# Optimization experiments

Hardware: AMD Instinct MI355X
Metric: run time of the kernel (lower is better)

## Reference

```python
import jax, jax.numpy as jnp
import numpy as np

EMBED_DIM = 64
CODEBOOK_SIZE = 1024
BETA = 0.25


def setup_inputs() -> dict:
    key = jax.random.key(0)
    k1, k2 = jax.random.split(key)
    inputs = jax.random.normal(k1, (32, 4096, EMBED_DIM), dtype=jnp.float32)
    lim = 1.0 / CODEBOOK_SIZE
    codebook = jax.random.uniform(k2, (CODEBOOK_SIZE, EMBED_DIM),
                                  minval=-lim, maxval=lim, dtype=jnp.float32)
    return {"inputs": inputs, "codebook": codebook}


def reference(inputs, codebook):
    orig_shape = inputs.shape
    flat = inputs.reshape(-1, EMBED_DIM)  # [N, D]
    d = (jnp.sum(flat * flat, axis=1, keepdims=True)
         - 2.0 * flat @ codebook.T
         + jnp.sum(codebook * codebook, axis=1)[None, :])
    codes = jnp.argmin(d, axis=1)                      # [N]
    quantized = codebook[codes].reshape(orig_shape)    # gather + reshape
    straight_through = inputs + jax.lax.stop_gradient(quantized - inputs)
    commitment = jnp.mean((inputs - jax.lax.stop_gradient(quantized)) ** 2)
    codebook_loss = jnp.mean((quantized - jax.lax.stop_gradient(inputs)) ** 2)
    loss = codebook_loss + BETA * commitment
    return straight_through, codes.reshape(orig_shape[:-1]), loss
```

## Files before the change

kernel.cpp:

```cpp
#include <hip/hip_runtime.h>

#define DIM   64
#define KCB   1024
#define RPB   256
#define QCAP  192
#define BCH   128

#define BSH_OFS 19988
#define SMEM_WORDS (BSH_OFS + BCH * 32)
#define SMEM_BYTES (SMEM_WORDS * 4)

#define WS_NEED_BYTES ((2048 + 32768) * 4)

typedef __attribute__((ext_vector_type(8))) short short8;
typedef __attribute__((ext_vector_type(4))) float f32x4;

__device__ __forceinline__ unsigned short f2bf(float f) {
    union { float f; unsigned u; } v; v.f = f;
    unsigned u = v.u;
    return (unsigned short)((u + 0x7FFFu + ((u >> 16) & 1u)) >> 16);
}

__global__ void vq_prep(const float* __restrict__ cb, float* __restrict__ ws, int do_bf) {
    int k = blockIdx.x * blockDim.x + threadIdx.x;
    if (k < KCB) {
        const float4* e4 = (const float4*)(cb + (k << 6));
        float4 xq[16];
        #pragma unroll
        for (int j = 0; j < 16; ++j) xq[j] = e4[j];
        {
            #pragma clang fp contract(off)
            float racc[8];
            racc[0]=xq[0].x*xq[0].x; racc[1]=xq[0].y*xq[0].y;
            racc[2]=xq[0].z*xq[0].z; racc[3]=xq[0].w*xq[0].w;
            racc[4]=xq[1].x*xq[1].x; racc[5]=xq[1].y*xq[1].y;
            racc[6]=xq[1].z*xq[1].z; racc[7]=xq[1].w*xq[1].w;
            #pragma unroll
            for (int t = 1; t < 8; ++t) {
                float4 a = xq[2*t], b = xq[2*t+1];
                racc[0]+=a.x*a.x; racc[1]+=a.y*a.y; racc[2]+=a.z*a.z; racc[3]+=a.w*a.w;
                racc[4]+=b.x*b.x; racc[5]+=b.y*b.y; racc[6]+=b.z*b.z; racc[7]+=b.w*b.w;
            }
            ws[256 + k] = ((racc[0] + racc[1]) + (racc[2] + racc[3]))
                        + ((racc[4] + racc[5]) + (racc[6] + racc[7]));
        }
        if (do_bf) {
            short8* dst = (short8*)((unsigned short*)(ws + 2048) + (k << 6));
            #pragma unroll
            for (int p = 0; p < 8; ++p) {
                float4 v = xq[2*p], u = xq[2*p+1];
                short8 s;
                s[0]=(short)f2bf(v.x); s[1]=(short)f2bf(v.y);
                s[2]=(short)f2bf(v.z); s[3]=(short)f2bf(v.w);
                s[4]=(short)f2bf(u.x); s[5]=(short)f2bf(u.y);
                s[6]=(short)f2bf(u.z); s[7]=(short)f2bf(u.w);
                dst[p] = s;
            }
        }
    }
    if (k == 0) ws[0] = 0.0f;
}

__global__ __launch_bounds__(1024, 1) void vq_mfma(
        const float* __restrict__ in,
        const float* __restrict__ cb,
        float* __restrict__ ws,
        float* __restrict__ codes_f,
        float* __restrict__ out)
{
    extern __shared__ float smem[];
    float* xs    = smem;
    float* Atab  = smem + 16384;
    float* Ttab  = smem + 16640;
    float* csq_s = smem + 16896;
    unsigned long long* keytab = (unsigned long long*)(smem + 17920);
    int* qcnt  = (int*)(smem + 18432);
    int* ovflp = (int*)(smem + 18448);
    unsigned short* qbuf = (unsigned short*)(smem + 18449);
    unsigned short* bsh  = (unsigned short*)(smem + BSH_OFS);

    const int tid  = threadIdx.x;
    const int lane = tid & 63;
    const int w    = tid >> 6;
    const int r    = lane & 15;
    const int g    = lane >> 4;
    const int wrow = w << 4;
    const size_t rowBase = (size_t)blockIdx.x * RPB;
    const float* csq = ws + 256;
    const unsigned short* cbh = (const unsigned short*)(ws + 2048);
    float* loss_acc = ws;

    {
        const float4* gx = (const float4*)(in + rowBase * DIM);
        #pragma unroll
        for (int i = 0; i < 4; ++i) {
            int idx = i * 1024 + tid;
            int row = idx >> 4, cj = idx & 15;
            float4 v = gx[idx];
            *(float4*)(xs + row * 64 + ((cj ^ (row & 15)) << 2)) = v;
        }
    }
    csq_s[tid] = csq[tid];
    if (tid < RPB) keytab[tid] = 0xFFFFFFFFFFFFFFFFull;
    if (tid < 16) qcnt[tid] = 0;
    if (tid == 0) *ovflp = 0;
    __syncthreads();

    if (tid < RPB) {
        const float* xr = xs + tid * 64;
        const int s = tid & 15;
        float A, S1;
        {
            #pragma clang fp contract(off)
            float racc[8], sacc[8];
            {
                float4 a = *(const float4*)(xr + ((0 ^ s) << 2));
                float4 b = *(const float4*)(xr + ((1 ^ s) << 2));
                racc[0]=a.x*a.x; racc[1]=a.y*a.y; racc[2]=a.z*a.z; racc[3]=a.w*a.w;
                racc[4]=b.x*b.x; racc[5]=b.y*b.y; racc[6]=b.z*b.z; racc[7]=b.w*b.w;
                sacc[0]=__builtin_fabsf(a.x); sacc[1]=__builtin_fabsf(a.y);
                sacc[2]=__builtin_fabsf(a.z); sacc[3]=__builtin_fabsf(a.w);
                sacc[4]=__builtin_fabsf(b.x); sacc[5]=__builtin_fabsf(b.y);
                sacc[6]=__builtin_fabsf(b.z); sacc[7]=__builtin_fabsf(b.w);
            }
            #pragma unroll
            for (int t = 1; t < 8; ++t) {
                float4 a = *(const float4*)(xr + (((2*t)   ^ s) << 2));
                float4 b = *(const float4*)(xr + (((2*t+1) ^ s) << 2));
                racc[0]+=a.x*a.x; racc[1]+=a.y*a.y; racc[2]+=a.z*a.z; racc[3]+=a.w*a.w;
                racc[4]+=b.x*b.x; racc[5]+=b.y*b.y; racc[6]+=b.z*b.z; racc[7]+=b.w*b.w;
                sacc[0]+=__builtin_fabsf(a.x); sacc[1]+=__builtin_fabsf(a.y);
                sacc[2]+=__builtin_fabsf(a.z); sacc[3]+=__builtin_fabsf(a.w);
                sacc[4]+=__builtin_fabsf(b.x); sacc[5]+=__builtin_fabsf(b.y);
                sacc[6]+=__builtin_fabsf(b.z); sacc[7]+=__builtin_fabsf(b.w);
            }
            A  = ((racc[0]+racc[1])+(racc[2]+racc[3]))
               + ((racc[4]+racc[5])+(racc[6]+racc[7]));
            S1 = ((sacc[0]+sacc[1])+(sacc[2]+sacc[3]))
               + ((sacc[4]+sacc[5])+(sacc[6]+sacc[7]));
        }
        Atab[tid] = A;
        Ttab[tid] = 1.52587890625e-05f * S1
                  + 4.76837158203125e-07f * (A + 1.0f)
                  + 1e-5f;
    }

    short8 af[2];
    #pragma unroll
    for (int h = 0; h < 2; ++h) {
        const int row = wrow + r;
        const int cj = h*8 + g*2;
        float4 v0 = *(const float4*)(xs + row*64 + (((cj  ) ^ r) << 2));
        float4 v1 = *(const float4*)(xs + row*64 + (((cj+1) ^ r) << 2));
        short8 a;
        a[0]=(short)f2bf(v0.x); a[1]=(short)f2bf(v0.y);
        a[2]=(short)f2bf(v0.z); a[3]=(short)f2bf(v0.w);
        a[4]=(short)f2bf(v1.x); a[5]=(short)f2bf(v1.y);
        a[6]=(short)f2bf(v1.z); a[7]=(short)f2bf(v1.w);
        af[h] = a;
    }

    const int sc = tid >> 3;
    const int sj = tid & 7;
    const int sdst = (sc << 6) + ((sj ^ (sc & 7)) << 3);

    float rm[4];
    #pragma unroll
    for (int s = 0; s < 4; ++s) rm[s] = -3.402823466e38f;

    #pragma unroll 1
    for (int nb = 0; nb < KCB; nb += BCH) {
        __syncthreads();
        *(short8*)(bsh + sdst) =
            *(const short8*)(cbh + ((nb + sc) << 6) + (sj << 3));
        __syncthreads();

        f32x4 acc[8];
        #pragma unroll
        for (int nt = 0; nt < 8; ++nt) {
            const float ch = -0.5f * csq_s[nb + nt*16 + r];
            f32x4 c; c[0]=ch; c[1]=ch; c[2]=ch; c[3]=ch;
            const unsigned short* bp = bsh + ((nt*16 + r) << 6);
            short8 b0 = *(const short8*)(bp + (((g    ) ^ (r & 7)) << 3));
            short8 b1 = *(const short8*)(bp + (((4 + g) ^ (r & 7)) << 3));
            c = __builtin_amdgcn_mfma_f32_16x16x32_bf16(af[0], b0, c, 0, 0, 0);
            c = __builtin_amdgcn_mfma_f32_16x16x32_bf16(af[1], b1, c, 0, 0, 0);
            acc[nt] = c;
        }

        #pragma unroll
        for (int rg = 0; rg < 4; ++rg) {
            float cm = fmaxf(fmaxf(fmaxf(acc[0][rg], acc[1][rg]),
                                   fmaxf(acc[2][rg], acc[3][rg])),
                             fmaxf(fmaxf(acc[4][rg], acc[5][rg]),
                                   fmaxf(acc[6][rg], acc[7][rg])));
            rm[rg] = fmaxf(rm[rg], cm);
        }
    }

    float thr[4];
    #pragma unroll
    for (int s = 0; s < 4; ++s) {
        float cm = rm[s];
        cm = fmaxf(cm, __shfl_xor(cm, 1));
        cm = fmaxf(cm, __shfl_xor(cm, 2));
        cm = fmaxf(cm, __shfl_xor(cm, 4));
        cm = fmaxf(cm, __shfl_xor(cm, 8));
        thr[s] = cm - Ttab[wrow + g*4 + s];
    }

    #pragma unroll 1
    for (int nb = 0; nb < KCB; nb += BCH) {
        __syncthreads();
        *(short8*)(bsh + sdst) =
            *(const short8*)(cbh + ((nb + sc) << 6) + (sj << 3));
        __syncthreads();

        f32x4 acc[8];
        #pragma unroll
        for (int nt = 0; nt < 8; ++nt) {
            const float ch = -0.5f * csq_s[nb + nt*16 + r];
            f32x4 c; c[0]=ch; c[1]=ch; c[2]=ch; c[3]=ch;
            const unsigned short* bp = bsh + ((nt*16 + r) << 6);
            short8 b0 = *(const short8*)(bp + (((g    ) ^ (r & 7)) << 3));
            short8 b1 = *(const short8*)(bp + (((4 + g) ^ (r & 7)) << 3));
            c = __builtin_amdgcn_mfma_f32_16x16x32_bf16(af[0], b0, c, 0, 0, 0);
            c = __builtin_amdgcn_mfma_f32_16x16x32_bf16(af[1], b1, c, 0, 0, 0);
            acc[nt] = c;
        }

        #pragma unroll
        for (int rg = 0; rg < 4; ++rg) {
            const float th = thr[rg];
            bool fl[8]; bool any = false;
            #pragma unroll
            for (int nt = 0; nt < 8; ++nt) { fl[nt] = acc[nt][rg] >= th; any |= fl[nt]; }
            if (__ballot(any)) {
                const int rowLocal = g*4 + rg;
                #pragma unroll
                for (int nt = 0; nt < 8; ++nt) {
                    unsigned long long m = __ballot(fl[nt]);
                    if (m) {
                        int base = 0;
                        if (lane == 0) base = atomicAdd(&qcnt[w], (int)__popcll(m));
                        base = __builtin_amdgcn_readfirstlane(base);
                        if (fl[nt]) {
                            int pos = base + (int)__popcll(m & ((1ull << lane) - 1ull));
                            if (pos < QCAP)
                                qbuf[w * QCAP + pos] =
                                    (unsigned short)((rowLocal << 10) | (nb + nt*16 + r));
                            else *ovflp = 1;
                        }
                    }
                }
            }
        }
    }

    const int cnt  = qcnt[w];
    const int cmax = cnt < QCAP ? cnt : QCAP;
    for (int base = 0; base < cmax; base += 64) {
        const int i = base + lane;
        if (i < cmax) {
            const int item = qbuf[w * QCAP + i];
            const int row = wrow + (item >> 10);
            const int n = item & 1023;
            const float* xr = xs + row * 64;
            const int sr = row & 15;
            const float4* e4 = (const float4*)(cb + ((size_t)n << 6));
            float mm = 0.f;
            #pragma unroll
            for (int j = 0; j < 16; ++j) {
                float4 xq = *(const float4*)(xr + ((j ^ sr) << 2));
                float4 eq = e4[j];
                mm = __builtin_fmaf(xq.x, eq.x, mm);
                mm = __builtin_fmaf(xq.y, eq.y, mm);
                mm = __builtin_fmaf(xq.z, eq.z, mm);
                mm = __builtin_fmaf(xq.w, eq.w, mm);
            }
            float dd;
            {
                #pragma clang fp contract(off)
                dd = (Atab[row] - 2.0f * mm) + csq_s[n];
            }
            unsigned long long key =
                ((unsigned long long)__float_as_uint(dd) << 32) | (unsigned)n;
            atomicMin(&keytab[row], key);
        }
    }
    __syncthreads();

    float* dtab = Ttab;
    if (tid < RPB) {
        unsigned long long kk = keytab[tid];
        int   kb = (int)(kk & 1023u);
        float db = __uint_as_float((unsigned)(kk >> 32));
        if (*ovflp) {
            const float* xr = in + (rowBase + tid) * (size_t)DIM;
            float dmin = 3.402823466e38f; int kmin = 0;
            for (int n = 0; n < KCB; ++n) {
                const float* eg = cb + ((size_t)n << 6);
                float mmv = 0.f;
                for (int j = 0; j < 64; ++j) mmv = __builtin_fmaf(xr[j], eg[j], mmv);
                float ddv;
                {
                    #pragma clang fp contract(off)
                    ddv = (Atab[tid] - 2.0f * mmv) + csq_s[n];
                }
                if (ddv < dmin) { dmin = ddv; kmin = n; }
            }
            db = dmin; kb = kmin;
        }
        dtab[tid] = db;
        codes_f[rowBase + tid] = (float)kb;
        keytab[tid] = (unsigned long long)(unsigned)kb;
    }
    __syncthreads();

    {
        float4* gout = (float4*)(out + rowBase * DIM);
        #pragma unroll
        for (int i = 0; i < 4; ++i) {
            int idx = i * 1024 + tid;
            int row = idx >> 4, cj = idx & 15;
            int code = (int)keytab[row];
            float4 qv = *(const float4*)(cb + ((size_t)code << 6) + (cj << 2));
            float4 xv = *(const float4*)(xs + row * 64 + ((cj ^ (row & 15)) << 2));
            float4 st;
            {
                #pragma clang fp contract(off)
                st.x = xv.x + (qv.x - xv.x);
                st.y = xv.y + (qv.y - xv.y);
                st.z = xv.z + (qv.z - xv.z);
                st.w = xv.w + (qv.w - xv.w);
            }
            gout[idx] = st;
        }
    }

    __syncthreads();
    #pragma unroll
    for (int s = 128; s > 0; s >>= 1) {
        if (tid < s) dtab[tid] += dtab[tid + s];
        __syncthreads();
    }
    if (tid == 0) atomicAdd(loss_acc, dtab[0]);
}

#define OLD_SMEM_WORDS 20480
#define OLD_SMEM_BYTES (OLD_SMEM_WORDS * 4)

__global__ __launch_bounds__(512, 4) void vq_main_old(
        const float* __restrict__ in,
        const float* __restrict__ cb,
        const float* __restrict__ csq,
        float* __restrict__ codes_f,
        float* __restrict__ out,
        float* __restrict__ loss_acc)
{
    extern __shared__ float smem[];
    float* xs    = smem;
    float* dtab  = smem + 16384;
    int*   ktab  = (int*)(smem + 18432);

    const int tid  = threadIdx.x;
    const int lane = tid & 63;
    const int q    = __builtin_amdgcn_readfirstlane(tid >> 6);
    const size_t rowBase = (size_t)blockIdx.x * RPB;

    {
        const float4* gx = (const float4*)(in + rowBase * DIM);
        #pragma unroll
        for (int i = 0; i < 8; ++i) {
            int idx = i * 512 + tid;
            int row = idx >> 4, cj = idx & 15;
            float4 v = gx[idx];
            *(float4*)(xs + row * 64 + ((cj ^ (row & 15)) << 2)) = v;
        }
    }
    __syncthreads();

    float A[4];
    #pragma unroll
    for (int ri = 0; ri < 4; ++ri) {
        const int row = lane + (ri << 6);
        float xv[64];
        #pragma unroll
        for (int cj = 0; cj < 16; ++cj) {
            float4 v = *(const float4*)(xs + row * 64 + ((cj ^ (lane & 15)) << 2));
            xv[cj*4+0]=v.x; xv[cj*4+1]=v.y; xv[cj*4+2]=v.z; xv[cj*4+3]=v.w;
        }
        {
            #pragma clang fp contract(off)
            float racc[8];
            #pragma unroll
            for (int j = 0; j < 8; ++j) racc[j] = xv[j] * xv[j];
            #pragma unroll
            for (int t = 1; t < 8; ++t) {
                #pragma unroll
                for (int j = 0; j < 8; ++j) racc[j] += xv[8*t+j] * xv[8*t+j];
            }
            A[ri] = ((racc[0] + racc[1]) + (racc[2] + racc[3]))
                  + ((racc[4] + racc[5]) + (racc[6] + racc[7]));
        }
    }

    const float* cbq   = cb  + ((size_t)q << 13);
    const float* csq_q = csq + (q << 7);
    float dmin[4] = {3.402823466e38f, 3.402823466e38f, 3.402823466e38f, 3.402823466e38f};
    int   kmin[4] = {0, 0, 0, 0};
    const int xb = lane * 64;

    #pragma unroll 1
    for (int ke = 0; ke < 128; ke += 16) {
        float m[4][16];
        #pragma unroll
        for (int ri = 0; ri < 4; ++ri)
            #pragma unroll
            for (int e = 0; e < 16; ++e) m[ri][e] = 0.0f;

        #pragma unroll 1
        for (int jb = 0; jb < 64; jb += 4) {
            const int slot4 = ((jb >> 2) ^ (lane & 15)) << 2;
            float4 a0 = *(const float4*)(xs + xb +         slot4);
            float4 a1 = *(const float4*)(xs + xb +  4096 + slot4);
            float4 a2 = *(const float4*)(xs + xb +  8192 + slot4);
            float4 a3 = *(const float4*)(xs + xb + 12288 + slot4);
            #pragma unroll
            for (int e = 0; e < 16; ++e) {
                float4 ev = *(const float4*)(cbq + ((ke + e) << 6) + jb);
                m[0][e] = __builtin_fmaf(a0.x, ev.x, m[0][e]);
                m[0][e] = __builtin_fmaf(a0.y, ev.y, m[0][e]);
                m[0][e] = __builtin_fmaf(a0.z, ev.z, m[0][e]);
                m[0][e] = __builtin_fmaf(a0.w, ev.w, m[0][e]);
                m[1][e] = __builtin_fmaf(a1.x, ev.x, m[1][e]);
                m[1][e] = __builtin_fmaf(a1.y, ev.y, m[1][e]);
                m[1][e] = __builtin_fmaf(a1.z, ev.z, m[1][e]);
                m[1][e] = __builtin_fmaf(a1.w, ev.w, m[1][e]);
                m[2][e] = __builtin_fmaf(a2.x, ev.x, m[2][e]);
                m[2][e] = __builtin_fmaf(a2.y, ev.y, m[2][e]);
                m[2][e] = __builtin_fmaf(a2.z, ev.z, m[2][e]);
                m[2][e] = __builtin_fmaf(a2.w, ev.w, m[2][e]);
                m[3][e] = __builtin_fmaf(a3.x, ev.x, m[3][e]);
                m[3][e] = __builtin_fmaf(a3.y, ev.y, m[3][e]);
                m[3][e] = __builtin_fmaf(a3.z, ev.z, m[3][e]);
                m[3][e] = __builtin_fmaf(a3.w, ev.w, m[3][e]);
            }
        }

        #pragma unroll
        for (int e = 0; e < 16; ++e) {
            float cse = csq_q[ke + e];
            int gk = (q << 7) + ke + e;
            #pragma unroll
            for (int ri = 0; ri < 4; ++ri) {
                float d;
                {
                    #pragma clang fp contract(off)
                    d = (A[ri] - 2.0f * m[ri][e]) + cse;
                }
                if (d < dmin[ri]) { dmin[ri] = d; kmin[ri] = gk; }
            }
        }
    }

    #pragma unroll
    for (int ri = 0; ri < 4; ++ri) {
        int row = lane + (ri << 6);
        dtab[row * 8 + q] = dmin[ri];
        ktab[row * 8 + q] = kmin[ri];
    }
    __syncthreads();

    float db = 0.0f;
    if (tid < RPB) {
        db = dtab[tid * 8];
        int kb = ktab[tid * 8];
        #pragma unroll
        for (int qq = 1; qq < 8; ++qq) {
            float dq = dtab[tid * 8 + qq];
            int   kq = ktab[tid * 8 + qq];
            if (dq < db) { db = dq; kb = kq; }
        }
        ktab[tid * 8] = kb;
        codes_f[rowBase + tid] = (float)kb;
    }
    __syncthreads();

    {
        float4* gout = (float4*)(out + rowBase * DIM);
        #pragma unroll
        for (int i = 0; i < 8; ++i) {
            int idx = i * 512 + tid;
            int row = idx >> 4, cj = idx & 15;
            int code = ktab[row * 8];
            float4 qv = *(const float4*)(cb + ((size_t)code << 6) + (cj << 2));
            float4 xv = *(const float4*)(xs + row * 64 + ((cj ^ (row & 15)) << 2));
            float4 st;
            {
                #pragma clang fp contract(off)
                st.x = xv.x + (qv.x - xv.x);
                st.y = xv.y + (qv.y - xv.y);
                st.z = xv.z + (qv.z - xv.z);
                st.w = xv.w + (qv.w - xv.w);
            }
            gout[idx] = st;
        }
    }

    if (tid < RPB) dtab[tid] = db;
    __syncthreads();
    #pragma unroll
    for (int s = 128; s > 0; s >>= 1) {
        if (tid < s) dtab[tid] += dtab[tid + s];
        __syncthreads();
    }
    if (tid == 0) atomicAdd(loss_acc, dtab[0]);
}

__global__ void vq_final(const float* __restrict__ ws, float* __restrict__ loss_out) {
    loss_out[0] = 1.25f * ws[0] / 8388608.0f;
}

extern "C" void kernel_launch(void* const* d_in, const int* in_sizes, int n_in,
                              void* d_out, int out_size, void* d_ws, size_t ws_size,
                              hipStream_t stream) {
    const float* in = (const float*)d_in[0];
    const float* cb = (const float*)d_in[1];
    float* out     = (float*)d_out;
    float* codes_f = out + 8388608;
    float* loss_p  = out + 8519680;
    float* ws      = (float*)d_ws;

    const int big = (ws_size >= (size_t)WS_NEED_BYTES) ? 1 : 0;

    vq_prep<<<16, 64, 0, stream>>>(cb, ws, big);
    if (big) {
        hipFuncSetAttribute((const void*)vq_mfma,
                            hipFuncAttributeMaxDynamicSharedMemorySize, SMEM_BYTES);
        vq_mfma<<<512, 1024, SMEM_BYTES, stream>>>(in, cb, ws, codes_f, out);
    } else {
        hipFuncSetAttribute((const void*)vq_main_old,
                            hipFuncAttributeMaxDynamicSharedMemorySize, OLD_SMEM_BYTES);
        vq_main_old<<<512, 512, OLD_SMEM_BYTES, stream>>>(in, cb, ws + 256, codes_f, out, ws);
    }
    vq_final<<<1, 1, 0, stream>>>(ws, loss_p);
}
```

Before: 161.1 us.

## Double-buffer codebook chunks in LDS with register prefetch and larger chunks

```diff
diff --git a/kernel.cpp b/kernel.cpp
--- a/kernel.cpp
+++ b/kernel.cpp
@@ -4,10 +4,12 @@
 #define KCB   1024
 #define RPB   256
 #define QCAP  192
-#define BCH   128
+#define BCH   256
+#define NCH   (KCB / BCH)
 
 #define BSH_OFS 19988
-#define SMEM_WORDS (BSH_OFS + BCH * 32)
+#define BUF_USH (BCH * 64)
+#define SMEM_WORDS (BSH_OFS + 2 * BCH * 32)
 #define SMEM_BYTES (SMEM_WORDS * 4)
 
 #define WS_NEED_BYTES ((2048 + 32768) * 4)
@@ -160,41 +162,53 @@
         af[h] = a;
     }
 
-    const int sc = tid >> 3;
-    const int sj = tid & 7;
-    const int sdst = (sc << 6) + ((sj ^ (sc & 7)) << 3);
+    const int c0 = tid >> 3,        j0 = tid & 7;
+    const int c1 = (tid + 1024) >> 3, j1 = tid & 7;
+    const int d0 = (c0 << 6) + ((j0 ^ (c0 & 7)) << 3);
+    const int d1 = (c1 << 6) + ((j1 ^ (c1 & 7)) << 3);
+
+    __syncthreads();
 
     float rm[4];
     #pragma unroll
     for (int s = 0; s < 4; ++s) rm[s] = -3.402823466e38f;
 
-    #pragma unroll 1
-    for (int nb = 0; nb < KCB; nb += BCH) {
+    {
+        short8 st0 = *(const short8*)(cbh + ((0 + c0) << 6) + (j0 << 3));
+        short8 st1 = *(const short8*)(cbh + ((0 + c1) << 6) + (j1 << 3));
+        *(short8*)(bsh + d0) = st0;
+        *(short8*)(bsh + d1) = st1;
         __syncthreads();
-        *(short8*)(bsh + sdst) =
-            *(const short8*)(cbh + ((nb + sc) << 6) + (sj << 3));
-        __syncthreads();
-
-        f32x4 acc[8];
-        #pragma unroll
-        for (int nt = 0; nt < 8; ++nt) {
-            const float ch = -0.5f * csq_s[nb + nt*16 + r];
-            f32x4 c; c[0]=ch; c[1]=ch; c[2]=ch; c[3]=ch;
-            const unsigned short* bp = bsh + ((nt*16 + r) << 6);
-            short8 b0 = *(const short8*)(bp + (((g    ) ^ (r & 7)) << 3));
-            short8 b1 = *(const short8*)(bp + (((4 + g) ^ (r & 7)) << 3));
-            c = __builtin_amdgcn_mfma_f32_16x16x32_bf16(af[0], b0, c, 0, 0, 0);
-            c = __builtin_amdgcn_mfma_f32_16x16x32_bf16(af[1], b1, c, 0, 0, 0);
-            acc[nt] = c;
-        }
-
-        #pragma unroll
-        for (int rg = 0; rg < 4; ++rg) {
-            float cm = fmaxf(fmaxf(fmaxf(acc[0][rg], acc[1][rg]),
-                                   fmaxf(acc[2][rg], acc[3][rg])),
-                             fmaxf(fmaxf(acc[4][rg], acc[5][rg]),
-                                   fmaxf(acc[6][rg], acc[7][rg])));
-            rm[rg] = fmaxf(rm[rg], cm);
+
+        #pragma unroll 1
+        for (int i = 0; i < NCH; ++i) {
+            const int nb = i * BCH;
+            const int cur = i & 1;
+            if (i < NCH - 1) {
+                st0 = *(const short8*)(cbh + ((nb + BCH + c0) << 6) + (j0 << 3));
+                st1 = *(const short8*)(cbh + ((nb + BCH + c1) << 6) + (j1 << 3));
+            }
+            const unsigned short* bb = bsh + cur * BUF_USH;
+            #pragma unroll
+            for (int nt = 0; nt < 16; ++nt) {
+                const float ch = -0.5f * csq_s[nb + nt*16 + r];
+                f32x4 c; c[0]=ch; c[1]=ch; c[2]=ch; c[3]=ch;
+                const unsigned short* bp = bb + ((nt*16 + r) << 6);
+                short8 b0 = *(const short8*)(bp + (((g    ) ^ (r & 7)) << 3));
+                short8 b1 = *(const short8*)(bp + (((4 + g) ^ (r & 7)) << 3));
+                c = __builtin_amdgcn_mfma_f32_16x16x32_bf16(af[0], b0, c, 0, 0, 0);
+                c = __builtin_amdgcn_mfma_f32_16x16x32_bf16(af[1], b1, c, 0, 0, 0);
+                rm[0] = fmaxf(rm[0], c[0]);
+                rm[1] = fmaxf(rm[1], c[1]);
+                rm[2] = fmaxf(rm[2], c[2]);
+                rm[3] = fmaxf(rm[3], c[3]);
+            }
+            if (i < NCH - 1) {
+                unsigned short* wb = bsh + (cur ^ 1) * BUF_USH;
+                *(short8*)(wb + d0) = st0;
+                *(short8*)(wb + d1) = st1;
+            }
+            __syncthreads();
         }
     }
 
@@ -209,51 +223,62 @@
         thr[s] = cm - Ttab[wrow + g*4 + s];
     }
 
-    #pragma unroll 1
-    for (int nb = 0; nb < KCB; nb += BCH) {
+    {
+        short8 st0 = *(const short8*)(cbh + ((0 + c0) << 6) + (j0 << 3));
+        short8 st1 = *(const short8*)(cbh + ((0 + c1) << 6) + (j1 << 3));
+        *(short8*)(bsh + d0) = st0;
+        *(short8*)(bsh + d1) = st1;
         __syncthreads();
-        *(short8*)(bsh + sdst) =
-            *(const short8*)(cbh + ((nb + sc) << 6) + (sj << 3));
-        __syncthreads();
-
-        f32x4 acc[8];
-        #pragma unroll
-        for (int nt = 0; nt < 8; ++nt) {
-            const float ch = -0.5f * csq_s[nb + nt*16 + r];
-            f32x4 c; c[0]=ch; c[1]=ch; c[2]=ch; c[3]=ch;
-            const unsigned short* bp = bsh + ((nt*16 + r) << 6);
-            short8 b0 = *(const short8*)(bp + (((g    ) ^ (r & 7)) << 3));
-            short8 b1 = *(const short8*)(bp + (((4 + g) ^ (r & 7)) << 3));
-            c = __builtin_amdgcn_mfma_f32_16x16x32_bf16(af[0], b0, c, 0, 0, 0);
-            c = __builtin_amdgcn_mfma_f32_16x16x32_bf16(af[1], b1, c, 0, 0, 0);
-            acc[nt] = c;
-        }
-
-        #pragma unroll
-        for (int rg = 0; rg < 4; ++rg) {
-            const float th = thr[rg];
-            bool fl[8]; bool any = false;
-            #pragma unroll
-            for (int nt = 0; nt < 8; ++nt) { fl[nt] = acc[nt][rg] >= th; any |= fl[nt]; }
-            if (__ballot(any)) {
-                const int rowLocal = g*4 + rg;
-                #pragma unroll
-                for (int nt = 0; nt < 8; ++nt) {
-                    unsigned long long m = __ballot(fl[nt]);
-                    if (m) {
-                        int base = 0;
-                        if (lane == 0) base = atomicAdd(&qcnt[w], (int)__popcll(m));
-                        base = __builtin_amdgcn_readfirstlane(base);
-                        if (fl[nt]) {
-                            int pos = base + (int)__popcll(m & ((1ull << lane) - 1ull));
-                            if (pos < QCAP)
-                                qbuf[w * QCAP + pos] =
-                                    (unsigned short)((rowLocal << 10) | (nb + nt*16 + r));
-                            else *ovflp = 1;
+
+        #pragma unroll 1
+        for (int i = 0; i < NCH; ++i) {
+            const int nb = i * BCH;
+            const int cur = i & 1;
+            if (i < NCH - 1) {
+                st0 = *(const short8*)(cbh + ((nb + BCH + c0) << 6) + (j0 << 3));
+                st1 = *(const short8*)(cbh + ((nb + BCH + c1) << 6) + (j1 << 3));
+            }
+            const unsigned short* bb = bsh + cur * BUF_USH;
+            #pragma unroll 1
+            for (int nt = 0; nt < 16; ++nt) {
+                const float ch = -0.5f * csq_s[nb + nt*16 + r];
+                f32x4 c; c[0]=ch; c[1]=ch; c[2]=ch; c[3]=ch;
+                const unsigned short* bp = bb + ((nt*16 + r) << 6);
+                short8 b0 = *(const short8*)(bp + (((g    ) ^ (r & 7)) << 3));
+                short8 b1 = *(const short8*)(bp + (((4 + g) ^ (r & 7)) << 3));
+                c = __builtin_amdgcn_mfma_f32_16x16x32_bf16(af[0], b0, c, 0, 0, 0);
+                c = __builtin_amdgcn_mfma_f32_16x16x32_bf16(af[1], b1, c, 0, 0, 0);
+                const bool f0 = c[0] >= thr[0];
+                const bool f1 = c[1] >= thr[1];
+                const bool f2 = c[2] >= thr[2];
+                const bool f3 = c[3] >= thr[3];
+                if (__ballot(f0 | f1 | f2 | f3)) {
+                    const int ent = nb + nt*16 + r;
+                    #pragma unroll
+                    for (int rg = 0; rg < 4; ++rg) {
+                        const bool fl = (rg==0)?f0:(rg==1)?f1:(rg==2)?f2:f3;
+                        unsigned long long m = __ballot(fl);
+                        if (m) {
+                            int base = 0;
+                            if (lane == 0) base = atomicAdd(&qcnt[w], (int)__popcll(m));
+                            base = __builtin_amdgcn_readfirstlane(base);
+                            if (fl) {
+                                int pos = base + (int)__popcll(m & ((1ull << lane) - 1ull));
+                                if (pos < QCAP)
+                                    qbuf[w * QCAP + pos] =
+                                        (unsigned short)(((g*4 + rg) << 10) | ent);
+                                else *ovflp = 1;
+                            }
                         }
                     }
                 }
             }
+            if (i < NCH - 1) {
+                unsigned short* wb = bsh + (cur ^ 1) * BUF_USH;
+                *(short8*)(wb + d0) = st0;
+                *(short8*)(wb + d1) = st1;
+            }
+            __syncthreads();
         }
     }
 
```

After: 161.4 us. Within noise of the previous version (+0.2%).

## Double-buffer codebook via direct global-to-LDS loads and split waves by rows and codebook halves

Applied to the files above, without the earlier changes.

```diff
diff --git a/kernel.cpp b/kernel.cpp
--- a/kernel.cpp
+++ b/kernel.cpp
@@ -4,10 +4,13 @@
 #define KCB   1024
 #define RPB   256
 #define QCAP  192
-#define BCH   128
-
-#define BSH_OFS 19988
-#define SMEM_WORDS (BSH_OFS + BCH * 32)
+#define BCH   256
+#define NCH   4
+
+#define RMT_OFS 19988
+#define BSH_OFS 20500
+#define BUF_USH (BCH * 64)
+#define SMEM_WORDS (BSH_OFS + 2 * BCH * 32)
 #define SMEM_BYTES (SMEM_WORDS * 4)
 
 #define WS_NEED_BYTES ((2048 + 32768) * 4)
@@ -19,6 +22,12 @@
     union { float f; unsigned u; } v; v.f = f;
     unsigned u = v.u;
     return (unsigned short)((u + 0x7FFFu + ((u >> 16) & 1u)) >> 16);
+}
+
+__device__ __forceinline__ void gload_lds16(const unsigned short* g, unsigned short* l) {
+    __builtin_amdgcn_global_load_lds(
+        (const __attribute__((address_space(1))) unsigned int*)g,
+        (__attribute__((address_space(3))) unsigned int*)l, 16, 0, 0);
 }
 
 __global__ void vq_prep(const float* __restrict__ cb, float* __restrict__ ws, int do_bf) {
@@ -77,14 +86,16 @@
     int* qcnt  = (int*)(smem + 18432);
     int* ovflp = (int*)(smem + 18448);
     unsigned short* qbuf = (unsigned short*)(smem + 18449);
-    unsigned short* bsh  = (unsigned short*)(smem + BSH_OFS);
+    float* rmtab = smem + RMT_OFS;
+    unsigned short* bsh = (unsigned short*)(smem + BSH_OFS);
 
     const int tid  = threadIdx.x;
     const int lane = tid & 63;
     const int w    = tid >> 6;
     const int r    = lane & 15;
     const int g    = lane >> 4;
-    const int wrow = w << 4;
+    const int half = w >> 3;
+    const int wrow2 = (w & 7) << 5;
     const size_t rowBase = (size_t)blockIdx.x * RPB;
     const float* csq = ws + 256;
     const unsigned short* cbh = (const unsigned short*)(ws + 2048);
@@ -145,116 +156,136 @@
                   + 1e-5f;
     }
 
-    short8 af[2];
-    #pragma unroll
-    for (int h = 0; h < 2; ++h) {
-        const int row = wrow + r;
-        const int cj = h*8 + g*2;
-        float4 v0 = *(const float4*)(xs + row*64 + (((cj  ) ^ r) << 2));
-        float4 v1 = *(const float4*)(xs + row*64 + (((cj+1) ^ r) << 2));
-        short8 a;
-        a[0]=(short)f2bf(v0.x); a[1]=(short)f2bf(v0.y);
-        a[2]=(short)f2bf(v0.z); a[3]=(short)f2bf(v0.w);
-        a[4]=(short)f2bf(v1.x); a[5]=(short)f2bf(v1.y);
-        a[6]=(short)f2bf(v1.z); a[7]=(short)f2bf(v1.w);
-        af[h] = a;
-    }
-
-    const int sc = tid >> 3;
-    const int sj = tid & 7;
-    const int sdst = (sc << 6) + ((sj ^ (sc & 7)) << 3);
-
-    float rm[4];
-    #pragma unroll
-    for (int s = 0; s < 4; ++s) rm[s] = -3.402823466e38f;
-
+    short8 af[2][2];
+    #pragma unroll
+    for (int mt = 0; mt < 2; ++mt)
+        #pragma unroll
+        for (int h = 0; h < 2; ++h) {
+            const int row = wrow2 + mt*16 + r;
+            const int cj = h*8 + g*2;
+            float4 v0 = *(const float4*)(xs + row*64 + (((cj  ) ^ r) << 2));
+            float4 v1 = *(const float4*)(xs + row*64 + (((cj+1) ^ r) << 2));
+            short8 a;
+            a[0]=(short)f2bf(v0.x); a[1]=(short)f2bf(v0.y);
+            a[2]=(short)f2bf(v0.z); a[3]=(short)f2bf(v0.w);
+            a[4]=(short)f2bf(v1.x); a[5]=(short)f2bf(v1.y);
+            a[6]=(short)f2bf(v1.z); a[7]=(short)f2bf(v1.w);
+            af[mt][h] = a;
+        }
+
+    const int c0  = tid >> 3;
+    const int gr0 = (tid & 7) ^ (c0 & 7);
+    #define STAGE_CHUNK(i_, buf_) do {                                          \
+        const unsigned short* _s = cbh + ((((i_) << 7) + c0) << 6) + (gr0 << 3);\
+        unsigned short* _d = bsh + (buf_) * BUF_USH + (tid << 3);               \
+        gload_lds16(_s, _d);                                                    \
+        gload_lds16(_s + (512 << 6), _d + 8192);                                \
+    } while (0)
+
+    float rm[8];
+    #pragma unroll
+    for (int s = 0; s < 8; ++s) rm[s] = -3.402823466e38f;
+
+    STAGE_CHUNK(0, 0);
+    __syncthreads();
     #pragma unroll 1
-    for (int nb = 0; nb < KCB; nb += BCH) {
-        __syncthreads();
-        *(short8*)(bsh + sdst) =
-            *(const short8*)(cbh + ((nb + sc) << 6) + (sj << 3));
-        __syncthreads();
-
-        f32x4 acc[8];
+    for (int i = 0; i < NCH; ++i) {
+        if (i < NCH - 1) STAGE_CHUNK(i + 1, (i & 1) ^ 1);
+        const unsigned short* bb = bsh + (i & 1) * BUF_USH;
+        const int nb128 = i << 7;
         #pragma unroll
         for (int nt = 0; nt < 8; ++nt) {
-            const float ch = -0.5f * csq_s[nb + nt*16 + r];
-            f32x4 c; c[0]=ch; c[1]=ch; c[2]=ch; c[3]=ch;
-            const unsigned short* bp = bsh + ((nt*16 + r) << 6);
+            const int ent = (half << 9) + nb128 + nt*16 + r;
+            const float ch = -0.5f * csq_s[ent];
+            f32x4 a0, a1;
+            a0[0]=ch; a0[1]=ch; a0[2]=ch; a0[3]=ch;
+            a1[0]=ch; a1[1]=ch; a1[2]=ch; a1[3]=ch;
+            const unsigned short* bp = bb + (((half << 7) + nt*16 + r) << 6);
             short8 b0 = *(const short8*)(bp + (((g    ) ^ (r & 7)) << 3));
             short8 b1 = *(const short8*)(bp + (((4 + g) ^ (r & 7)) << 3));
-            c = __builtin_amdgcn_mfma_f32_16x16x32_bf16(af[0], b0, c, 0, 0, 0);
-            c = __builtin_amdgcn_mfma_f32_16x16x32_bf16(af[1], b1, c, 0, 0, 0);
-            acc[nt] = c;
-        }
-
-        #pragma unroll
-        for (int rg = 0; rg < 4; ++rg) {
-            float cm = fmaxf(fmaxf(fmaxf(acc[0][rg], acc[1][rg]),
-                                   fmaxf(acc[2][rg], acc[3][rg])),
-                             fmaxf(fmaxf(acc[4][rg], acc[5][rg]),
-                                   fmaxf(acc[6][rg], acc[7][rg])));
-            rm[rg] = fmaxf(rm[rg], cm);
-        }
-    }
-
-    float thr[4];
-    #pragma unroll
-    for (int s = 0; s < 4; ++s) {
+            a0 = __builtin_amdgcn_mfma_f32_16x16x32_bf16(af[0][0], b0, a0, 0, 0, 0);
+            a0 = __builtin_amdgcn_mfma_f32_16x16x32_bf16(af[0][1], b1, a0, 0, 0, 0);
+            a1 = __builtin_amdgcn_mfma_f32_16x16x32_bf16(af[1][0], b0, a1, 0, 0, 0);
+            a1 = __builtin_amdgcn_mfma_f32_16x16x32_bf16(af[1][1], b1, a1, 0, 0, 0);
+            rm[0]=fmaxf(rm[0],a0[0]); rm[1]=fmaxf(rm[1],a0[1]);
+            rm[2]=fmaxf(rm[2],a0[2]); rm[3]=fmaxf(rm[3],a0[3]);
+            rm[4]=fmaxf(rm[4],a1[0]); rm[5]=fmaxf(rm[5],a1[1]);
+            rm[6]=fmaxf(rm[6],a1[2]); rm[7]=fmaxf(rm[7],a1[3]);
+        }
+        __syncthreads();
+    }
+
+    #pragma unroll
+    for (int s = 0; s < 8; ++s) {
         float cm = rm[s];
         cm = fmaxf(cm, __shfl_xor(cm, 1));
         cm = fmaxf(cm, __shfl_xor(cm, 2));
         cm = fmaxf(cm, __shfl_xor(cm, 4));
         cm = fmaxf(cm, __shfl_xor(cm, 8));
-        thr[s] = cm - Ttab[wrow + g*4 + s];
+        rm[s] = cm;
+    }
+    if (r == 0) {
+        #pragma unroll
+        for (int s = 0; s < 8; ++s) {
+            const int row = wrow2 + (s >> 2)*16 + g*4 + (s & 3);
+            rmtab[row * 2 + half] = rm[s];
+        }
+    }
+    STAGE_CHUNK(0, 0);
+    __syncthreads();
+    float thr[8];
+    #pragma unroll
+    for (int s = 0; s < 8; ++s) {
+        const int row = wrow2 + (s >> 2)*16 + g*4 + (s & 3);
+        thr[s] = fmaxf(rmtab[row * 2], rmtab[row * 2 + 1]) - Ttab[row];
     }
 
     #pragma unroll 1
-    for (int nb = 0; nb < KCB; nb += BCH) {
-        __syncthreads();
-        *(short8*)(bsh + sdst) =
-            *(const short8*)(cbh + ((nb + sc) << 6) + (sj << 3));
-        __syncthreads();
-
-        f32x4 acc[8];
-        #pragma unroll
+    for (int i = 0; i < NCH; ++i) {
+        if (i < NCH - 1) STAGE_CHUNK(i + 1, (i & 1) ^ 1);
+        const unsigned short* bb = bsh + (i & 1) * BUF_USH;
+        const int nb128 = i << 7;
+        #pragma unroll 1
         for (int nt = 0; nt < 8; ++nt) {
-            const float ch = -0.5f * csq_s[nb + nt*16 + r];
-            f32x4 c; c[0]=ch; c[1]=ch; c[2]=ch; c[3]=ch;
-            const unsigned short* bp = bsh + ((nt*16 + r) << 6);
+            const int ent = (half << 9) + nb128 + nt*16 + r;
+            const float ch = -0.5f * csq_s[ent];
+            f32x4 a0, a1;
+            a0[0]=ch; a0[1]=ch; a0[2]=ch; a0[3]=ch;
+            a1[0]=ch; a1[1]=ch; a1[2]=ch; a1[3]=ch;
+            const unsigned short* bp = bb + (((half << 7) + nt*16 + r) << 6);
             short8 b0 = *(const short8*)(bp + (((g    ) ^ (r & 7)) << 3));
             short8 b1 = *(const short8*)(bp + (((4 + g) ^ (r & 7)) << 3));
-            c = __builtin_amdgcn_mfma_f32_16x16x32_bf16(af[0], b0, c, 0, 0, 0);
-            c = __builtin_amdgcn_mfma_f32_16x16x32_bf16(af[1], b1, c, 0, 0, 0);
-            acc[nt] = c;
-        }
-
-        #pragma unroll
-        for (int rg = 0; rg < 4; ++rg) {
-            const float th = thr[rg];
-            bool fl[8]; bool any = false;
-            #pragma unroll
-            for (int nt = 0; nt < 8; ++nt) { fl[nt] = acc[nt][rg] >= th; any |= fl[nt]; }
+            a0 = __builtin_amdgcn_mfma_f32_16x16x32_bf16(af[0][0], b0, a0, 0, 0, 0);
+            a0 = __builtin_amdgcn_mfma_f32_16x16x32_bf16(af[0][1], b1, a0, 0, 0, 0);
+            a1 = __builtin_amdgcn_mfma_f32_16x16x32_bf16(af[1][0], b0, a1, 0, 0, 0);
+            a1 = __builtin_amdgcn_mfma_f32_16x16x32_bf16(af[1][1], b1, a1, 0, 0, 0);
+            bool fl[8];
+            fl[0]=a0[0]>=thr[0]; fl[1]=a0[1]>=thr[1];
+            fl[2]=a0[2]>=thr[2]; fl[3]=a0[3]>=thr[3];
+            fl[4]=a1[0]>=thr[4]; fl[5]=a1[1]>=thr[5];
+            fl[6]=a1[2]>=thr[6]; fl[7]=a1[3]>=thr[7];
+            bool any = fl[0]|fl[1]|fl[2]|fl[3]|fl[4]|fl[5]|fl[6]|fl[7];
             if (__ballot(any)) {
-                const int rowLocal = g*4 + rg;
                 #pragma unroll
-                for (int nt = 0; nt < 8; ++nt) {
-                    unsigned long long m = __ballot(fl[nt]);
+                for (int s = 0; s < 8; ++s) {
+                    unsigned long long m = __ballot(fl[s]);
                     if (m) {
                         int base = 0;
                         if (lane == 0) base = atomicAdd(&qcnt[w], (int)__popcll(m));
                         base = __builtin_amdgcn_readfirstlane(base);
-                        if (fl[nt]) {
+                        if (fl[s]) {
+                            const int rowLocal = (s >> 2)*16 + g*4 + (s & 3);
                             int pos = base + (int)__popcll(m & ((1ull << lane) - 1ull));
                             if (pos < QCAP)
                                 qbuf[w * QCAP + pos] =
-                                    (unsigned short)((rowLocal << 10) | (nb + nt*16 + r));
+                                    (unsigned short)((rowLocal << 10) | ent);
                             else *ovflp = 1;
                         }
                     }
                 }
             }
         }
+        __syncthreads();
     }
 
     const int cnt  = qcnt[w];
@@ -263,7 +294,7 @@
         const int i = base + lane;
         if (i < cmax) {
             const int item = qbuf[w * QCAP + i];
-            const int row = wrow + (item >> 10);
+            const int row = wrow2 + (item >> 10);
             const int n = item & 1023;
             const float* xr = xs + row * 64;
             const int sr = row & 15;
```

Result: faster. 152.1 us (-5.6%).
